# Kernel optimization log

Hardware: AMD Instinct MI355X
Metric: run time of the kernel (lower is better)

## Reference

```python
import jax, jax.numpy as jnp
import numpy as np

HID, H, D = 128, 4, 32
NB, NP, NC = 60000, 2000, 4000
EM, EP, EI = 150000, 300000, 150000


def segment_softmax(logits, seg, n):
    # logits: [E, H], seg: [E] destination ids
    m = jax.ops.segment_max(logits, seg, num_segments=n)
    m = jnp.where(jnp.isfinite(m), m, 0.0)  # guard empty segments
    e = jnp.exp(logits - m[seg])
    s = jax.ops.segment_sum(e, seg, num_segments=n)
    return e / (s[seg] + 1e-16)


def layer_norm(x, g, b):
    mu = x.mean(-1, keepdims=True)
    v = ((x - mu) ** 2).mean(-1, keepdims=True)
    return (x - mu) / jnp.sqrt(v + 1e-5) * g + b


def setup_inputs():
    key = jax.random.key(0)
    ks = jax.random.split(key, 40)
    i = iter(range(40))
    nrm = lambda shape, s=1.0: jax.random.normal(ks[next(i)], shape, jnp.float32) * s
    w = lambda shape: nrm(shape, 0.05)
    inp = {
        'x_ball': nrm((NB, HID)),
        'x_player': nrm((NP, HID)),
        'x_context': nrm((NC, HID)),
        'em': jnp.stack([jax.random.randint(ks[next(i)], (EM,), 0, NP),
                         jax.random.randint(ks[next(i)], (EM,), 0, NB)]),
        'ep': jnp.stack([jax.random.randint(ks[next(i)], (EP,), 0, NB),
                         jax.random.randint(ks[next(i)], (EP,), 0, NB)]),
        'ei': jnp.stack([jax.random.randint(ks[next(i)], (EI,), 0, NB),
                         jax.random.randint(ks[next(i)], (EI,), 0, NC)]),
        'ea_p': nrm((EP, 1)),
        # GATv2Conv (player -matchup-> ball)
        'g_Wl': w((HID, HID)), 'g_Wr': w((HID, HID)), 'g_att': w((H, D)), 'g_b': jnp.zeros((HID,), jnp.float32),
        # TransformerConv (ball -recent_precedes-> ball), edge_dim=1
        't_Wq': w((HID, HID)), 't_bq': jnp.zeros((HID,), jnp.float32),
        't_Wk': w((HID, HID)), 't_bk': jnp.zeros((HID,), jnp.float32),
        't_Wv': w((HID, HID)), 't_bv': jnp.zeros((HID,), jnp.float32),
        't_We': w((1, HID)),
        't_Wskip': w((HID, HID)), 't_bskip': jnp.zeros((HID,), jnp.float32),
        # SAGEConv mean (ball -informs-> context)
        's_Wl': w((HID, HID)), 's_bl': jnp.zeros((HID,), jnp.float32), 's_Wr': w((HID, HID)),
        # per-type LayerNorms (only applied to types produced by the conv)
        'ln_ball_g': jnp.ones((HID,), jnp.float32), 'ln_ball_b': jnp.zeros((HID,), jnp.float32),
        'ln_ctx_g': jnp.ones((HID,), jnp.float32), 'ln_ctx_b': jnp.zeros((HID,), jnp.float32),
    }
    return inp


def reference(x_ball, x_player, x_context, em, ep, ei, ea_p,
              g_Wl, g_Wr, g_att, g_b,
              t_Wq, t_bq, t_Wk, t_bk, t_Wv, t_bv, t_We, t_Wskip, t_bskip,
              s_Wl, s_bl, s_Wr,
              ln_ball_g, ln_ball_b, ln_ctx_g, ln_ctx_b):
    # ---- GATv2Conv: player -> ball ----
    src, dst = em[0], em[1]
    xl = (x_player @ g_Wl).reshape(NP, H, D)   # src transform
    xr = (x_ball @ g_Wr).reshape(NB, H, D)     # dst transform
    e = xl[src] + xr[dst]                      # [EM, H, D]
    e = jnp.where(e > 0, e, 0.2 * e)           # leaky_relu(0.2)
    logit = jnp.einsum('ehd,hd->eh', e, g_att)
    alpha = segment_softmax(logit, dst, NB)
    gat = jax.ops.segment_sum(xl[src] * alpha[..., None], dst, num_segments=NB)
    gat = gat.reshape(NB, HID) + g_b

    # ---- TransformerConv: ball -> ball, edge_dim=1 ----
    src, dst = ep[0], ep[1]
    q = (x_ball @ t_Wq + t_bq).reshape(NB, H, D)
    k = (x_ball @ t_Wk + t_bk).reshape(NB, H, D)
    v = (x_ball @ t_Wv + t_bv).reshape(NB, H, D)
    ee = (ea_p @ t_We).reshape(EP, H, D)       # lin_edge (no bias)
    kj = k[src] + ee
    logit = jnp.einsum('ehd,ehd->eh', q[dst], kj) / jnp.sqrt(jnp.float32(D))
    alpha = segment_softmax(logit, dst, NB)
    tr = jax.ops.segment_sum((v[src] + ee) * alpha[..., None], dst, num_segments=NB)
    tr = tr.reshape(NB, HID) + x_ball @ t_Wskip + t_bskip  # root/skip connection

    # ---- SAGEConv mean: ball -> context ----
    src, dst = ei[0], ei[1]
    summ = jax.ops.segment_sum(x_ball[src], dst, num_segments=NC)
    cnt = jax.ops.segment_sum(jnp.ones((EI,), jnp.float32), dst, num_segments=NC)
    mean = summ / jnp.maximum(cnt, 1.0)[:, None]
    sage = mean @ s_Wl + s_bl + x_context @ s_Wr

    # ---- HeteroConv aggr='sum' + residual + per-type LayerNorm ----
    ball_out = layer_norm(gat + tr + x_ball, ln_ball_g, ln_ball_b)
    ctx_out = layer_norm(sage + x_context, ln_ctx_g, ln_ctx_b)
    # 'player' receives no messages -> passed through unchanged
    return (ball_out, ctx_out, x_player)
```

## Files before the change

### kernel.cpp

```cpp
#include <hip/hip_runtime.h>
#include <hip/hip_bf16.h>

#define NB 60000
#define NP 2000
#define NC 4000
#define EM_N 150000
#define EP_N 300000
#define EI_N 150000
#define POOL_N (EM_N + EP_N + EI_N)
#define SEG_TOT (NB + NB + NC)
#define SCAN_BLK 1024
#define NPART ((SEG_TOT + SCAN_BLK - 1) / SCAN_BLK)
#define BALL_BLKS ((NB + 127) / 128)
#define PLYR_BLKS ((NP + 127) / 128)
#define GEMM_BLKS (BALL_BLKS + PLYR_BLKS)
#define FILL_BLKS ((POOL_N + 255) / 256)
#define BBALL ((NB + 3) / 4)
#define COPY_BLKS ((NP * 128 + 255) / 256)

typedef __hip_bfloat16 bf16;
typedef unsigned int u32;
typedef __attribute__((ext_vector_type(8))) short s8v;
typedef __attribute__((ext_vector_type(4))) float f4v;

__device__ __forceinline__ short f2bs(float f) {
    bf16 h = __float2bfloat16(f);
    return __builtin_bit_cast(short, h);
}
__device__ __forceinline__ float bsToF(short s) {
    return __builtin_bit_cast(float, ((unsigned)(unsigned short)s) << 16);
}
__device__ __forceinline__ float loF(u32 v) { return bsToF((short)(v & 0xffff)); }
__device__ __forceinline__ float hiF(u32 v) { return bsToF((short)(v >> 16)); }
__device__ __forceinline__ u32 packbf(float a, float b) {
    return (u32)(unsigned short)f2bs(a) | ((u32)(unsigned short)f2bs(b) << 16);
}

__global__ void hist_wt_kernel(const int* __restrict__ em, const int* __restrict__ ep,
                               const int* __restrict__ ei, int* __restrict__ counts,
                               const float* __restrict__ W0, const float* __restrict__ W1,
                               const float* __restrict__ W2, const float* __restrict__ W3,
                               const float* __restrict__ W4, const float* __restrict__ W5,
                               ushort* __restrict__ Wt) {
    int t = blockIdx.x * 256 + threadIdx.x;
    if (t < 6 * 16384) {
        int w = t >> 14, r = t & 16383, k = r >> 7, n = r & 127;
        const float* W = (w == 0) ? W0 : (w == 1) ? W1 : (w == 2) ? W2 : (w == 3) ? W3
                       : (w == 4) ? W4 : W5;
        int sc = (n >> 5) * 32 + ((n & 1) << 4) + ((n & 31) >> 1);
        Wt[w * 16384 + sc * 128 + k] = (unsigned short)f2bs(W[k * 128 + n]);
    }
    if (t < EM_N) atomicAdd(&counts[em[EM_N + t]], 1);
    else if (t < EM_N + EP_N) atomicAdd(&counts[NB + ep[EP_N + (t - EM_N)]], 1);
    else if (t < POOL_N) atomicAdd(&counts[2 * NB + ei[EI_N + (t - EM_N - EP_N)]], 1);
}

__global__ void scan_fused_kernel(const int* __restrict__ counts, int* __restrict__ offsets,
                                  int* __restrict__ cursors, int* __restrict__ gbase) {
    __shared__ int sd[256];
    __shared__ int sbase;
    int b = blockIdx.x, tid = threadIdx.x;
    int base = b * SCAN_BLK + tid * 4;
    int v[4]; int ts = 0;
#pragma unroll
    for (int j = 0; j < 4; j++) { int idx = base + j; v[j] = (idx < SEG_TOT) ? counts[idx] : 0; ts += v[j]; }
    sd[tid] = ts;
    for (int off = 1; off < 256; off <<= 1) {
        __syncthreads(); int t = (tid >= off) ? sd[tid - off] : 0;
        __syncthreads(); sd[tid] += t;
    }
    __syncthreads();
    if (tid == 255) sbase = atomicAdd(gbase, sd[255]);
    __syncthreads();
    int run = sd[tid] - ts + sbase;
#pragma unroll
    for (int j = 0; j < 4; j++) {
        int idx = base + j;
        if (idx < SEG_TOT) { offsets[idx] = run; cursors[idx] = run; }
        run += v[j];
    }
}

__global__ __launch_bounds__(256) void gemm6_fill_kernel(
    const float* __restrict__ Aball, const float* __restrict__ Aplyr,
    const ushort* __restrict__ Wt,
    const float* __restrict__ bq, const float* __restrict__ bk,
    const float* __restrict__ bv_, const float* __restrict__ bskip,
    u32* __restrict__ xrP, u32* __restrict__ qP, u32* __restrict__ kvP,
    u32* __restrict__ skipP, u32* __restrict__ xlP,
    const int* __restrict__ em, const int* __restrict__ ep, const int* __restrict__ ei,
    const float* __restrict__ ea_p, int* __restrict__ cursors, int2* __restrict__ pool) {
    if (blockIdx.x >= GEMM_BLKS) {
        int t = (blockIdx.x - GEMM_BLKS) * 256 + threadIdx.x;
        int seg, s; float ea = 0.f;
        if (t < EM_N) { s = em[t]; seg = em[EM_N + t]; }
        else if (t < EM_N + EP_N) { int e = t - EM_N; s = ep[e]; seg = NB + ep[EP_N + e]; ea = ea_p[e]; }
        else if (t < POOL_N) { int e = t - EM_N - EP_N; s = ei[e]; seg = 2 * NB + ei[EI_N + e]; }
        else return;
        int pos = atomicAdd(&cursors[seg], 1);
        pool[pos] = make_int2(s, __float_as_int(ea));
        return;
    }
    const int lane = threadIdx.x & 63;
    const int wv = threadIdx.x >> 6;
    const int quad = lane >> 4, l16 = lane & 15;
    const bool plyr = (blockIdx.x >= BALL_BLKS);
    const int M = plyr ? NP : NB;
    const float* A = plyr ? Aplyr : Aball;
    const int mbase = (plyr ? (blockIdx.x - BALL_BLKS) : blockIdx.x) * 128 + wv * 32;

    s8v a[2][4];
#pragma unroll
    for (int mt = 0; mt < 2; mt++) {
        int row = mbase + mt * 16 + l16;
        if (row >= M) row = M - 1;
        const float* ap = A + (size_t)row * 128 + quad * 8;
#pragma unroll
        for (int kt = 0; kt < 4; kt++) {
            const float4* p = (const float4*)(ap + kt * 32);
            float4 u = p[0], v = p[1];
            s8v f;
            f[0] = f2bs(u.x); f[1] = f2bs(u.y); f[2] = f2bs(u.z); f[3] = f2bs(u.w);
            f[4] = f2bs(v.x); f[5] = f2bs(v.y); f[6] = f2bs(v.z); f[7] = f2bs(v.w);
            a[mt][kt] = f;
        }
    }

    const int wbeg = plyr ? 5 : 0, wend = plyr ? 6 : 5;
    for (int w = wbeg; w < wend; w++) {
        const ushort* wt = Wt + w * 16384;
        u32* op; const float* bp; int stride, obase;
        if (w == 0)      { op = xrP;   bp = nullptr; stride = 64;  obase = 0; }
        else if (w == 1) { op = qP;    bp = bq;      stride = 64;  obase = 0; }
        else if (w == 2) { op = kvP;   bp = bk;      stride = 128; obase = 0; }
        else if (w == 3) { op = kvP;   bp = bv_;     stride = 128; obase = 1; }
        else if (w == 4) { op = skipP; bp = bskip;   stride = 64;  obase = 0; }
        else             { op = xlP;   bp = nullptr; stride = 64;  obase = 0; }
        const int kvmul = (stride == 128) ? 2 : 1;
#pragma unroll
        for (int t = 0; t < 4; t++) {
            s8v blo[4], bhi[4];
#pragma unroll
            for (int kt = 0; kt < 4; kt++) {
                blo[kt] = *(const s8v*)(wt + (t * 32 + l16) * 128 + kt * 32 + quad * 8);
                bhi[kt] = *(const s8v*)(wt + (t * 32 + 16 + l16) * 128 + kt * 32 + quad * 8);
            }
            float bvlo = 0.f, bvhi = 0.f;
            if (bp) { float2 b2 = ((const float2*)bp)[t * 16 + l16]; bvlo = b2.x; bvhi = b2.y; }
#pragma unroll
            for (int mt = 0; mt < 2; mt++) {
                f4v alo = {0.f, 0.f, 0.f, 0.f}, ahi = {0.f, 0.f, 0.f, 0.f};
#pragma unroll
                for (int kt = 0; kt < 4; kt++) {
                    alo = __builtin_amdgcn_mfma_f32_16x16x32_bf16(a[mt][kt], blo[kt], alo, 0, 0, 0);
                    ahi = __builtin_amdgcn_mfma_f32_16x16x32_bf16(a[mt][kt], bhi[kt], ahi, 0, 0, 0);
                }
#pragma unroll
                for (int r = 0; r < 4; r++) {
                    int row = mbase + mt * 16 + quad * 4 + r;
                    if (row < M)
                        op[(size_t)row * stride + (t * 16 + l16) * kvmul + obase]
                            = packbf(alo[r] + bvlo, ahi[r] + bvhi);
                }
            }
        }
    }
}

__global__ __launch_bounds__(256) void ball_sage_copy_kernel(
    const u32* __restrict__ xlP, const u32* __restrict__ xrP, const u32* __restrict__ qP,
    const u32* __restrict__ kvP, const u32* __restrict__ skipP,
    const float* __restrict__ x_ball, const float* __restrict__ x_player,
    const float* __restrict__ g_att, const float* __restrict__ g_b,
    const float* __restrict__ We,
    const int* __restrict__ offsets, const int* __restrict__ counts,
    const int2* __restrict__ pool,
    const float* __restrict__ ln_g, const float* __restrict__ ln_b,
    float* __restrict__ summ, float* __restrict__ out) {
    __shared__ float part[4][128];
    const int wv = threadIdx.x >> 6, l = threadIdx.x & 63;

    if (blockIdx.x >= BBALL + NC) {
        int t = (blockIdx.x - BBALL - NC) * 256 + threadIdx.x;
        if (t < NP * 128) out[(size_t)(NB + NC) * 128 + t] = x_player[t];
        return;
    }
    if (blockIdx.x >= BBALL) {
        int c = blockIdx.x - BBALL;
        int beg = offsets[2 * NB + c], cnt = counts[2 * NB + c];
        float s0 = 0.f, s1 = 0.f;
        for (int j = wv; j < cnt; j += 4) {
            int s = pool[beg + j].x;
            float2 xv = ((const float2*)x_ball)[(size_t)s * 64 + l];
            s0 += xv.x; s1 += xv.y;
        }
        part[wv][l * 2] = s0; part[wv][l * 2 + 1] = s1;
        __syncthreads();
        if (wv == 0) {
            float m = fmaxf((float)cnt, 1.f);
            size_t rowC = (size_t)c * 128;
            summ[rowC + l * 2] = (part[0][l * 2] + part[1][l * 2] + part[2][l * 2] + part[3][l * 2]) / m;
            summ[rowC + l * 2 + 1] =
                (part[0][l * 2 + 1] + part[1][l * 2 + 1] + part[2][l * 2 + 1] + part[3][l * 2 + 1]) / m;
        }
        return;
    }

    const int d = blockIdx.x * 4 + wv;
    if (d >= NB) return;
    const size_t rowD = (size_t)d * 64;

    float2 att = ((const float2*)g_att)[l];
    u32 xr2 = xrP[rowD + l];
    float xr0 = loF(xr2), xr1 = hiF(xr2);
    int beg = offsets[d], cnt = counts[d];
    float n0 = 0.f, n1 = 0.f, deg = 0.f;
    int j = 0;
    for (; j + 3 < cnt; j += 4) {
        int s0 = pool[beg + j].x, s1 = pool[beg + j + 1].x;
        int s2 = pool[beg + j + 2].x, s3 = pool[beg + j + 3].x;
        u32 xv0 = xlP[(size_t)s0 * 64 + l], xv1 = xlP[(size_t)s1 * 64 + l];
        u32 xv2 = xlP[(size_t)s2 * 64 + l], xv3 = xlP[(size_t)s3 * 64 + l];
        float p[4], xa[4], xb[4];
        u32 xv[4] = {xv0, xv1, xv2, xv3};
#pragma unroll
        for (int i = 0; i < 4; i++) {
            xa[i] = loF(xv[i]); xb[i] = hiF(xv[i]);
            float u0 = xa[i] + xr0; u0 = u0 > 0.f ? u0 : 0.2f * u0;
            float u1 = xb[i] + xr1; u1 = u1 > 0.f ? u1 : 0.2f * u1;
            p[i] = u0 * att.x + u1 * att.y;
        }
#pragma unroll
        for (int m = 1; m <= 8; m <<= 1) {
#pragma unroll
            for (int i = 0; i < 4; i++) p[i] += __shfl_xor(p[i], m);
        }
#pragma unroll
        for (int i = 0; i < 4; i++) {
            p[i] = __expf(p[i]);
            n0 += p[i] * xa[i]; n1 += p[i] * xb[i]; deg += p[i];
        }
    }
    for (; j < cnt; j++) {
        int s = pool[beg + j].x;
        u32 xv = xlP[(size_t)s * 64 + l];
        float x0 = loF(xv), x1 = hiF(xv);
        float u0 = x0 + xr0; u0 = u0 > 0.f ? u0 : 0.2f * u0;
        float u1 = x1 + xr1; u1 = u1 > 0.f ? u1 : 0.2f * u1;
        float p = u0 * att.x + u1 * att.y;
#pragma unroll
        for (int m = 1; m <= 8; m <<= 1) p += __shfl_xor(p, m);
        p = __expf(p);
        n0 += p * x0; n1 += p * x1; deg += p;
    }
    float gat0 = n0 / (deg + 1e-16f), gat1 = n1 / (deg + 1e-16f);

    u32 q2 = qP[rowD + l];
    float q0 = loF(q2), q1 = hiF(q2);
    float2 we = ((const float2*)We)[l];
    float dw = q0 * we.x + q1 * we.y;
#pragma unroll
    for (int m = 1; m <= 8; m <<= 1) dw += __shfl_xor(dw, m);
    beg = offsets[NB + d]; cnt = counts[NB + d];
    float sv0 = 0.f, sv1 = 0.f, spe = 0.f, det = 0.f;
    const uint2* kv2p = (const uint2*)kvP;
    j = 0;
    for (; j + 3 < cnt; j += 4) {
        int2 pr[4] = {pool[beg + j], pool[beg + j + 1], pool[beg + j + 2], pool[beg + j + 3]};
        uint2 kv[4];
#pragma unroll
        for (int i = 0; i < 4; i++) kv[i] = kv2p[(size_t)pr[i].x * 64 + l];
        float p[4], ea[4];
#pragma unroll
        for (int i = 0; i < 4; i++) {
            ea[i] = __int_as_float(pr[i].y);
            p[i] = q0 * loF(kv[i].x) + q1 * hiF(kv[i].x);
        }
#pragma unroll
        for (int m = 1; m <= 8; m <<= 1) {
#pragma unroll
            for (int i = 0; i < 4; i++) p[i] += __shfl_xor(p[i], m);
        }
#pragma unroll
        for (int i = 0; i < 4; i++) {
            p[i] = __expf((p[i] + ea[i] * dw) * 0.17677669529663687f);
            sv0 += p[i] * loF(kv[i].y); sv1 += p[i] * hiF(kv[i].y);
            spe += p[i] * ea[i]; det += p[i];
        }
    }
    for (; j < cnt; j++) {
        int2 pr = pool[beg + j];
        float ea = __int_as_float(pr.y);
        uint2 kv = kv2p[(size_t)pr.x * 64 + l];
        float p = q0 * loF(kv.x) + q1 * hiF(kv.x);
#pragma unroll
        for (int m = 1; m <= 8; m <<= 1) p += __shfl_xor(p, m);
        p = __expf((p + ea * dw) * 0.17677669529663687f);
        sv0 += p * loF(kv.y); sv1 += p * hiF(kv.y);
        spe += p * ea; det += p;
    }
    float tr0 = (sv0 + spe * we.x) / (det + 1e-16f);
    float tr1 = (sv1 + spe * we.y) / (det + 1e-16f);

    u32 sk = skipP[rowD + l];
    float2 xb2 = ((const float2*)x_ball)[rowD + l];
    float2 gb2 = ((const float2*)g_b)[l];
    float val0 = loF(sk) + gat0 + tr0 + xb2.x + gb2.x;
    float val1 = hiF(sk) + gat1 + tr1 + xb2.y + gb2.y;
    float s = val0 + val1;
#pragma unroll
    for (int m = 1; m <= 32; m <<= 1) s += __shfl_xor(s, m);
    float mu = s * (1.f / 128.f);
    float d0 = val0 - mu, d1 = val1 - mu;
    float qv = d0 * d0 + d1 * d1;
#pragma unroll
    for (int m = 1; m <= 32; m <<= 1) qv += __shfl_xor(qv, m);
    float inv = rsqrtf(qv * (1.f / 128.f) + 1e-5f);
    float2 g2 = ((const float2*)ln_g)[l];
    float2 b2 = ((const float2*)ln_b)[l];
    ((float2*)out)[rowD + l] = make_float2(d0 * inv * g2.x + b2.x, d1 * inv * g2.y + b2.y);
}

__global__ void ctx_fused_kernel(const float* __restrict__ xc, const float* __restrict__ summ,
                                 const float* __restrict__ Wr, const float* __restrict__ Wl,
                                 const float* __restrict__ bl,
                                 const float* __restrict__ g, const float* __restrict__ b,
                                 float* __restrict__ out) {
    __shared__ float A0[16 * 128];
    __shared__ float A1[16 * 128];
    __shared__ float CB[16 * 128];
    const int tid = threadIdx.x;
    const int row0 = blockIdx.x * 16;
    for (int i = tid; i < 16 * 128; i += 256) {
        int r = row0 + (i >> 7);
        A0[i] = (r < NC) ? xc[(size_t)r * 128 + (i & 127)] : 0.f;
        A1[i] = (r < NC) ? summ[(size_t)r * 128 + (i & 127)] : 0.f;
    }
    __syncthreads();
    const int col = tid & 127, rg = tid >> 7;
    float acc[8];
#pragma unroll
    for (int i = 0; i < 8; i++) acc[i] = 0.f;
    for (int k = 0; k < 128; k++) {
        float w0 = Wr[k * 128 + col], w1 = Wl[k * 128 + col];
#pragma unroll
        for (int i = 0; i < 8; i++)
            acc[i] += A0[(rg * 8 + i) * 128 + k] * w0 + A1[(rg * 8 + i) * 128 + k] * w1;
    }
    float bv = bl[col];
#pragma unroll
    for (int i = 0; i < 8; i++)
        CB[(rg * 8 + i) * 128 + col] = acc[i] + bv + A0[(rg * 8 + i) * 128 + col];
    __syncthreads();
    const int wv = tid >> 6, l = tid & 63;
    for (int r = 0; r < 4; r++) {
        int lr = wv * 4 + r, row = row0 + lr;
        if (row >= NC) break;
        float v0 = CB[lr * 128 + l], v1 = CB[lr * 128 + l + 64];
        float s = v0 + v1;
#pragma unroll
        for (int m = 1; m <= 32; m <<= 1) s += __shfl_xor(s, m);
        float mu = s * (1.f / 128.f);
        float d0 = v0 - mu, d1 = v1 - mu;
        float qv = d0 * d0 + d1 * d1;
#pragma unroll
        for (int m = 1; m <= 32; m <<= 1) qv += __shfl_xor(qv, m);
        float inv = rsqrtf(qv * (1.f / 128.f) + 1e-5f);
        out[(size_t)row * 128 + l] = d0 * inv * g[l] + b[l];
        out[(size_t)row * 128 + l + 64] = d1 * inv * g[l + 64] + b[l + 64];
    }
}

extern "C" void kernel_launch(void* const* d_in, const int* in_sizes, int n_in,
                              void* d_out, int out_size, void* d_ws, size_t ws_size,
                              hipStream_t stream) {
    const float* x_ball = (const float*)d_in[0];
    const float* x_player = (const float*)d_in[1];
    const float* x_context = (const float*)d_in[2];
    const int* em = (const int*)d_in[3];
    const int* ep = (const int*)d_in[4];
    const int* ei = (const int*)d_in[5];
    const float* ea_p = (const float*)d_in[6];
    const float* g_Wl = (const float*)d_in[7];
    const float* g_Wr = (const float*)d_in[8];
    const float* g_att = (const float*)d_in[9];
    const float* g_b = (const float*)d_in[10];
    const float* t_Wq = (const float*)d_in[11];
    const float* t_bq = (const float*)d_in[12];
    const float* t_Wk = (const float*)d_in[13];
    const float* t_bk = (const float*)d_in[14];
    const float* t_Wv = (const float*)d_in[15];
    const float* t_bv = (const float*)d_in[16];
    const float* t_We = (const float*)d_in[17];
    const float* t_Wskip = (const float*)d_in[18];
    const float* t_bskip = (const float*)d_in[19];
    const float* s_Wl = (const float*)d_in[20];
    const float* s_bl = (const float*)d_in[21];
    const float* s_Wr = (const float*)d_in[22];
    const float* ln_ball_g = (const float*)d_in[23];
    const float* ln_ball_b = (const float*)d_in[24];
    const float* ln_ctx_g = (const float*)d_in[25];
    const float* ln_ctx_b = (const float*)d_in[26];
    float* out = (float*)d_out;

    float* ws = (float*)d_ws;
    size_t o = 0;
    float* summ = ws + o;           o += (size_t)NC * 128;
    int* counts = (int*)(ws + o);   o += SEG_TOT;
    int* gbase = (int*)(ws + o);    o += 1;
    int* offsets = (int*)(ws + o);  o += SEG_TOT;
    int* cursors = (int*)(ws + o);  o += SEG_TOT;
    if (o & 1) o++;
    int2* pool = (int2*)(ws + o);   o += (size_t)POOL_N * 2;
    ushort* Wt = (ushort*)(ws + o); o += (6 * 16384) / 2;
    u32* xlP = (u32*)(ws + o);      o += (size_t)NP * 64;
    u32* xrP = (u32*)(ws + o);      o += (size_t)NB * 64;
    u32* qP = (u32*)(ws + o);       o += (size_t)NB * 64;
    u32* skipP = (u32*)(ws + o);    o += (size_t)NB * 64;
    if (o & 1) o++;
    u32* kvP = (u32*)(ws + o);      o += (size_t)NB * 128;

    dim3 blk(256);
    hipMemsetAsync(counts, 0, (SEG_TOT + 1) * sizeof(int), stream);
    hist_wt_kernel<<<(POOL_N + 255) / 256, blk, 0, stream>>>(em, ep, ei, counts,
                                                             g_Wr, t_Wq, t_Wk, t_Wv, t_Wskip, g_Wl, Wt);
    scan_fused_kernel<<<NPART, blk, 0, stream>>>(counts, offsets, cursors, gbase);
    gemm6_fill_kernel<<<GEMM_BLKS + FILL_BLKS, blk, 0, stream>>>(
        x_ball, x_player, Wt, t_bq, t_bk, t_bv, t_bskip, xrP, qP, kvP, skipP, xlP,
        em, ep, ei, ea_p, cursors, pool);
    ball_sage_copy_kernel<<<BBALL + NC + COPY_BLKS, blk, 0, stream>>>(
        xlP, xrP, qP, kvP, skipP, x_ball, x_player, g_att, g_b, t_We,
        offsets, counts, pool, ln_ball_g, ln_ball_b, summ, out);
    ctx_fused_kernel<<<(NC + 15) / 16, blk, 0, stream>>>(x_context, summ, s_Wr, s_Wl, s_bl,
                                                         ln_ctx_g, ln_ctx_b, out + (size_t)NB * 128);
}
```

Before: 332.3 us.

## Fuse SAGE aggregation into context GEMM kernel and fold residual into skip GEMM

Merges the context mean-aggregation and the context linear+LayerNorm into one block per 16 context rows, which removes the separate ctx kernel launch and the summ workspace round trip. The player passthrough copy moves into the histogram kernel. The x_ball residual and GAT bias are added in the skip GEMM epilogue, so the ball kernel no longer reads x_ball per row. In exchange, the residual is now rounded to bf16 in skipP, which adds precision loss, and the context blocks carry a serial gather followed by a scalar GEMM.

```diff
diff --git a/kernel.cpp b/kernel.cpp
--- a/kernel.cpp
+++ b/kernel.cpp
@@ -15,8 +15,9 @@
 #define PLYR_BLKS ((NP + 127) / 128)
 #define GEMM_BLKS (BALL_BLKS + PLYR_BLKS)
 #define FILL_BLKS ((POOL_N + 255) / 256)
+#define COPY_BLKS ((NP * 128 + 255) / 256)
 #define BBALL ((NB + 3) / 4)
-#define COPY_BLKS ((NP * 128 + 255) / 256)
+#define CTX_BLKS ((NC + 15) / 16)
 
 typedef __hip_bfloat16 bf16;
 typedef unsigned int u32;
@@ -36,12 +37,18 @@
     return (u32)(unsigned short)f2bs(a) | ((u32)(unsigned short)f2bs(b) << 16);
 }
 
-__global__ void hist_wt_kernel(const int* __restrict__ em, const int* __restrict__ ep,
-                               const int* __restrict__ ei, int* __restrict__ counts,
-                               const float* __restrict__ W0, const float* __restrict__ W1,
-                               const float* __restrict__ W2, const float* __restrict__ W3,
-                               const float* __restrict__ W4, const float* __restrict__ W5,
-                               ushort* __restrict__ Wt) {
+__global__ void hist_wt_copy_kernel(const int* __restrict__ em, const int* __restrict__ ep,
+                                    const int* __restrict__ ei, int* __restrict__ counts,
+                                    const float* __restrict__ W0, const float* __restrict__ W1,
+                                    const float* __restrict__ W2, const float* __restrict__ W3,
+                                    const float* __restrict__ W4, const float* __restrict__ W5,
+                                    ushort* __restrict__ Wt,
+                                    const float* __restrict__ x_player, float* __restrict__ out) {
+    if (blockIdx.x >= FILL_BLKS) {
+        int t = (blockIdx.x - FILL_BLKS) * 256 + threadIdx.x;
+        if (t < NP * 128) out[(size_t)(NB + NC) * 128 + t] = x_player[t];
+        return;
+    }
     int t = blockIdx.x * 256 + threadIdx.x;
     if (t < 6 * 16384) {
         int w = t >> 14, r = t & 16383, k = r >> 7, n = r & 127;
@@ -86,6 +93,7 @@
     const ushort* __restrict__ Wt,
     const float* __restrict__ bq, const float* __restrict__ bk,
     const float* __restrict__ bv_, const float* __restrict__ bskip,
+    const float* __restrict__ g_b,
     u32* __restrict__ xrP, u32* __restrict__ qP, u32* __restrict__ kvP,
     u32* __restrict__ skipP, u32* __restrict__ xlP,
     const int* __restrict__ em, const int* __restrict__ ep, const int* __restrict__ ei,
@@ -137,6 +145,7 @@
         else if (w == 4) { op = skipP; bp = bskip;   stride = 64;  obase = 0; }
         else             { op = xlP;   bp = nullptr; stride = 64;  obase = 0; }
         const int kvmul = (stride == 128) ? 2 : 1;
+        const bool resid = (w == 4);
 #pragma unroll
         for (int t = 0; t < 4; t++) {
             s8v blo[4], bhi[4];
@@ -147,6 +156,7 @@
             }
             float bvlo = 0.f, bvhi = 0.f;
             if (bp) { float2 b2 = ((const float2*)bp)[t * 16 + l16]; bvlo = b2.x; bvhi = b2.y; }
+            if (resid) { float2 gb2 = ((const float2*)g_b)[t * 16 + l16]; bvlo += gb2.x; bvhi += gb2.y; }
 #pragma unroll
             for (int mt = 0; mt < 2; mt++) {
                 f4v alo = {0.f, 0.f, 0.f, 0.f}, ahi = {0.f, 0.f, 0.f, 0.f};
@@ -158,50 +168,95 @@
 #pragma unroll
                 for (int r = 0; r < 4; r++) {
                     int row = mbase + mt * 16 + quad * 4 + r;
-                    if (row < M)
-                        op[(size_t)row * stride + (t * 16 + l16) * kvmul + obase]
-                            = packbf(alo[r] + bvlo, ahi[r] + bvhi);
+                    if (row < M) {
+                        float vlo = alo[r] + bvlo, vhi = ahi[r] + bvhi;
+                        if (resid) {
+                            float2 xr2 = ((const float2*)Aball)[(size_t)row * 64 + t * 16 + l16];
+                            vlo += xr2.x; vhi += xr2.y;
+                        }
+                        op[(size_t)row * stride + (t * 16 + l16) * kvmul + obase] = packbf(vlo, vhi);
+                    }
                 }
             }
         }
     }
 }
 
-__global__ __launch_bounds__(256) void ball_sage_copy_kernel(
+__global__ __launch_bounds__(256) void ball_ctx_kernel(
     const u32* __restrict__ xlP, const u32* __restrict__ xrP, const u32* __restrict__ qP,
     const u32* __restrict__ kvP, const u32* __restrict__ skipP,
-    const float* __restrict__ x_ball, const float* __restrict__ x_player,
-    const float* __restrict__ g_att, const float* __restrict__ g_b,
-    const float* __restrict__ We,
+    const float* __restrict__ x_ball, const float* __restrict__ xc,
+    const float* __restrict__ g_att, const float* __restrict__ We,
     const int* __restrict__ offsets, const int* __restrict__ counts,
     const int2* __restrict__ pool,
     const float* __restrict__ ln_g, const float* __restrict__ ln_b,
-    float* __restrict__ summ, float* __restrict__ out) {
-    __shared__ float part[4][128];
+    const float* __restrict__ Wr, const float* __restrict__ Wl, const float* __restrict__ bl,
+    const float* __restrict__ cg, const float* __restrict__ cb,
+    float* __restrict__ out) {
+    __shared__ float A0[16 * 128];
+    __shared__ float CB[16 * 128];
     const int wv = threadIdx.x >> 6, l = threadIdx.x & 63;
 
-    if (blockIdx.x >= BBALL + NC) {
-        int t = (blockIdx.x - BBALL - NC) * 256 + threadIdx.x;
-        if (t < NP * 128) out[(size_t)(NB + NC) * 128 + t] = x_player[t];
-        return;
-    }
     if (blockIdx.x >= BBALL) {
-        int c = blockIdx.x - BBALL;
-        int beg = offsets[2 * NB + c], cnt = counts[2 * NB + c];
-        float s0 = 0.f, s1 = 0.f;
-        for (int j = wv; j < cnt; j += 4) {
-            int s = pool[beg + j].x;
-            float2 xv = ((const float2*)x_ball)[(size_t)s * 64 + l];
-            s0 += xv.x; s1 += xv.y;
-        }
-        part[wv][l * 2] = s0; part[wv][l * 2 + 1] = s1;
+        const int tid = threadIdx.x;
+        const int row0 = (blockIdx.x - BBALL) * 16;
+        for (int i = tid; i < 16 * 128; i += 256) {
+            int r = row0 + (i >> 7);
+            A0[i] = (r < NC) ? xc[(size_t)r * 128 + (i & 127)] : 0.f;
+        }
+        for (int rr = 0; rr < 4; rr++) {
+            int n = wv * 4 + rr, c = row0 + n;
+            float s0 = 0.f, s1 = 0.f; int cnt = 0;
+            if (c < NC) {
+                int beg = offsets[2 * NB + c]; cnt = counts[2 * NB + c];
+                int j = 0;
+                for (; j + 1 < cnt; j += 2) {
+                    int sA = pool[beg + j].x, sB = pool[beg + j + 1].x;
+                    float2 xa = ((const float2*)x_ball)[(size_t)sA * 64 + l];
+                    float2 xb = ((const float2*)x_ball)[(size_t)sB * 64 + l];
+                    s0 += xa.x + xb.x; s1 += xa.y + xb.y;
+                }
+                if (j < cnt) {
+                    float2 xv = ((const float2*)x_ball)[(size_t)pool[beg + j].x * 64 + l];
+                    s0 += xv.x; s1 += xv.y;
+                }
+            }
+            float m = fmaxf((float)cnt, 1.f);
+            CB[n * 128 + 2 * l] = s0 / m;
+            CB[n * 128 + 2 * l + 1] = s1 / m;
+        }
         __syncthreads();
-        if (wv == 0) {
-            float m = fmaxf((float)cnt, 1.f);
-            size_t rowC = (size_t)c * 128;
-            summ[rowC + l * 2] = (part[0][l * 2] + part[1][l * 2] + part[2][l * 2] + part[3][l * 2]) / m;
-            summ[rowC + l * 2 + 1] =
-                (part[0][l * 2 + 1] + part[1][l * 2 + 1] + part[2][l * 2 + 1] + part[3][l * 2 + 1]) / m;
+        const int col = tid & 127, rg = tid >> 7;
+        float acc[8];
+#pragma unroll
+        for (int i = 0; i < 8; i++) acc[i] = 0.f;
+        for (int k = 0; k < 128; k++) {
+            float w0 = Wr[k * 128 + col], w1 = Wl[k * 128 + col];
+#pragma unroll
+            for (int i = 0; i < 8; i++)
+                acc[i] += A0[(rg * 8 + i) * 128 + k] * w0 + CB[(rg * 8 + i) * 128 + k] * w1;
+        }
+        float bv = bl[col];
+        __syncthreads();
+#pragma unroll
+        for (int i = 0; i < 8; i++)
+            CB[(rg * 8 + i) * 128 + col] = acc[i] + bv + A0[(rg * 8 + i) * 128 + col];
+        __syncthreads();
+        for (int r = 0; r < 4; r++) {
+            int lr = wv * 4 + r, row = row0 + lr;
+            if (row >= NC) break;
+            float v0 = CB[lr * 128 + l], v1 = CB[lr * 128 + l + 64];
+            float s = v0 + v1;
+#pragma unroll
+            for (int m = 1; m <= 32; m <<= 1) s += __shfl_xor(s, m);
+            float mu = s * (1.f / 128.f);
+            float d0 = v0 - mu, d1 = v1 - mu;
+            float qv = d0 * d0 + d1 * d1;
+#pragma unroll
+            for (int m = 1; m <= 32; m <<= 1) qv += __shfl_xor(qv, m);
+            float inv = rsqrtf(qv * (1.f / 128.f) + 1e-5f);
+            out[(size_t)(NB + row) * 128 + l] = d0 * inv * cg[l] + cb[l];
+            out[(size_t)(NB + row) * 128 + l + 64] = d1 * inv * cg[l + 64] + cb[l + 64];
         }
         return;
     }
@@ -219,10 +274,9 @@
     for (; j + 3 < cnt; j += 4) {
         int s0 = pool[beg + j].x, s1 = pool[beg + j + 1].x;
         int s2 = pool[beg + j + 2].x, s3 = pool[beg + j + 3].x;
-        u32 xv0 = xlP[(size_t)s0 * 64 + l], xv1 = xlP[(size_t)s1 * 64 + l];
-        u32 xv2 = xlP[(size_t)s2 * 64 + l], xv3 = xlP[(size_t)s3 * 64 + l];
+        u32 xv[4] = {xlP[(size_t)s0 * 64 + l], xlP[(size_t)s1 * 64 + l],
+                     xlP[(size_t)s2 * 64 + l], xlP[(size_t)s3 * 64 + l]};
         float p[4], xa[4], xb[4];
-        u32 xv[4] = {xv0, xv1, xv2, xv3};
 #pragma unroll
         for (int i = 0; i < 4; i++) {
             xa[i] = loF(xv[i]); xb[i] = hiF(xv[i]);
@@ -303,10 +357,8 @@
     float tr1 = (sv1 + spe * we.y) / (det + 1e-16f);
 
     u32 sk = skipP[rowD + l];
-    float2 xb2 = ((const float2*)x_ball)[rowD + l];
-    float2 gb2 = ((const float2*)g_b)[l];
-    float val0 = loF(sk) + gat0 + tr0 + xb2.x + gb2.x;
-    float val1 = hiF(sk) + gat1 + tr1 + xb2.y + gb2.y;
+    float val0 = loF(sk) + gat0 + tr0;
+    float val1 = hiF(sk) + gat1 + tr1;
     float s = val0 + val1;
 #pragma unroll
     for (int m = 1; m <= 32; m <<= 1) s += __shfl_xor(s, m);
@@ -319,56 +371,6 @@
     float2 g2 = ((const float2*)ln_g)[l];
     float2 b2 = ((const float2*)ln_b)[l];
     ((float2*)out)[rowD + l] = make_float2(d0 * inv * g2.x + b2.x, d1 * inv * g2.y + b2.y);
-}
-
-__global__ void ctx_fused_kernel(const float* __restrict__ xc, const float* __restrict__ summ,
-                                 const float* __restrict__ Wr, const float* __restrict__ Wl,
-                                 const float* __restrict__ bl,
-                                 const float* __restrict__ g, const float* __restrict__ b,
-                                 float* __restrict__ out) {
-    __shared__ float A0[16 * 128];
-    __shared__ float A1[16 * 128];
-    __shared__ float CB[16 * 128];
-    const int tid = threadIdx.x;
-    const int row0 = blockIdx.x * 16;
-    for (int i = tid; i < 16 * 128; i += 256) {
-        int r = row0 + (i >> 7);
-        A0[i] = (r < NC) ? xc[(size_t)r * 128 + (i & 127)] : 0.f;
-        A1[i] = (r < NC) ? summ[(size_t)r * 128 + (i & 127)] : 0.f;
-    }
-    __syncthreads();
-    const int col = tid & 127, rg = tid >> 7;
-    float acc[8];
-#pragma unroll
-    for (int i = 0; i < 8; i++) acc[i] = 0.f;
-    for (int k = 0; k < 128; k++) {
-        float w0 = Wr[k * 128 + col], w1 = Wl[k * 128 + col];
-#pragma unroll
-        for (int i = 0; i < 8; i++)
-            acc[i] += A0[(rg * 8 + i) * 128 + k] * w0 + A1[(rg * 8 + i) * 128 + k] * w1;
-    }
-    float bv = bl[col];
-#pragma unroll
-    for (int i = 0; i < 8; i++)
-        CB[(rg * 8 + i) * 128 + col] = acc[i] + bv + A0[(rg * 8 + i) * 128 + col];
-    __syncthreads();
-    const int wv = tid >> 6, l = tid & 63;
-    for (int r = 0; r < 4; r++) {
-        int lr = wv * 4 + r, row = row0 + lr;
-        if (row >= NC) break;
-        float v0 = CB[lr * 128 + l], v1 = CB[lr * 128 + l + 64];
-        float s = v0 + v1;
-#pragma unroll
-        for (int m = 1; m <= 32; m <<= 1) s += __shfl_xor(s, m);
-        float mu = s * (1.f / 128.f);
-        float d0 = v0 - mu, d1 = v1 - mu;
-        float qv = d0 * d0 + d1 * d1;
-#pragma unroll
-        for (int m = 1; m <= 32; m <<= 1) qv += __shfl_xor(qv, m);
-        float inv = rsqrtf(qv * (1.f / 128.f) + 1e-5f);
-        out[(size_t)row * 128 + l] = d0 * inv * g[l] + b[l];
-        out[(size_t)row * 128 + l + 64] = d1 * inv * g[l + 64] + b[l + 64];
-    }
 }
 
 extern "C" void kernel_launch(void* const* d_in, const int* in_sizes, int n_in,
@@ -405,7 +407,6 @@
 
     float* ws = (float*)d_ws;
     size_t o = 0;
-    float* summ = ws + o;           o += (size_t)NC * 128;
     int* counts = (int*)(ws + o);   o += SEG_TOT;
     int* gbase = (int*)(ws + o);    o += 1;
     int* offsets = (int*)(ws + o);  o += SEG_TOT;
@@ -422,15 +423,14 @@
 
     dim3 blk(256);
     hipMemsetAsync(counts, 0, (SEG_TOT + 1) * sizeof(int), stream);
-    hist_wt_kernel<<<(POOL_N + 255) / 256, blk, 0, stream>>>(em, ep, ei, counts,
-                                                             g_Wr, t_Wq, t_Wk, t_Wv, t_Wskip, g_Wl, Wt);
+    hist_wt_copy_kernel<<<FILL_BLKS + COPY_BLKS, blk, 0, stream>>>(
+        em, ep, ei, counts, g_Wr, t_Wq, t_Wk, t_Wv, t_Wskip, g_Wl, Wt, x_player, out);
     scan_fused_kernel<<<NPART, blk, 0, stream>>>(counts, offsets, cursors, gbase);
     gemm6_fill_kernel<<<GEMM_BLKS + FILL_BLKS, blk, 0, stream>>>(
-        x_ball, x_player, Wt, t_bq, t_bk, t_bv, t_bskip, xrP, qP, kvP, skipP, xlP,
-        em, ep, ei, ea_p, cursors, pool);
-    ball_sage_copy_kernel<<<BBALL + NC + COPY_BLKS, blk, 0, stream>>>(
-        xlP, xrP, qP, kvP, skipP, x_ball, x_player, g_att, g_b, t_We,
-        offsets, counts, pool, ln_ball_g, ln_ball_b, summ, out);
-    ctx_fused_kernel<<<(NC + 15) / 16, blk, 0, stream>>>(x_context, summ, s_Wr, s_Wl, s_bl,
-                                                         ln_ctx_g, ln_ctx_b, out + (size_t)NB * 128);
-}
+        x_ball, x_player, Wt, t_bq, t_bk, t_bv, t_bskip, g_b,
+        xrP, qP, kvP, skipP, xlP, em, ep, ei, ea_p, cursors, pool);
+    ball_ctx_kernel<<<BBALL + CTX_BLKS, blk, 0, stream>>>(
+        xlP, xrP, qP, kvP, skipP, x_ball, x_context, g_att, t_We,
+        offsets, counts, pool, ln_ball_g, ln_ball_b,
+        s_Wr, s_Wl, s_bl, ln_ctx_g, ln_ctx_b, out);
+}
```

Measured after the change: 364.4 us. +9.6%, slower.
